# Performance work log

Hardware: AMD Instinct MI355X
Metric: run time of the kernel (lower is better)

## Reference

```python
import jax, jax.numpy as jnp
import numpy as np
import math

N = 8192
F_DIM = 128
ALPHA_SLOPE = 0.2  # LeakyReLU negative slope from __init__ alpha


def setup_inputs() -> dict:
    key = jax.random.key(0)
    k1, k2, k3, k4, k5 = jax.random.split(key, 5)
    inp = jax.random.normal(k1, (N, F_DIM), dtype=jnp.float32)
    adj = (jax.random.uniform(k2, (N, N)) < 0.02).astype(jnp.float32)
    adj = adj.at[jnp.arange(N), jnp.arange(N)].set(1.0)
    h0 = jax.random.normal(k3, (N, F_DIM), dtype=jnp.float32)
    W = jax.random.normal(k4, (F_DIM, F_DIM), dtype=jnp.float32) * (1.414 * math.sqrt(6.0 / (2 * F_DIM)))
    a = jax.random.normal(k5, (2 * F_DIM, 1), dtype=jnp.float32) * (1.414 * math.sqrt(6.0 / (2 * F_DIM + 1)))
    return {"inp": inp, "adj": adj, "h0": h0, "W": W, "a": a,
            "lamda": 0.5, "alpha_mix": 0.1, "l": 1}


def reference(inp, adj, h0, W, a, lamda, alpha_mix, l):
    # h = inp @ W  -> (N, F)
    h = inp @ W
    # score(i,j) = leakyrelu([h_i, h_j] @ a) = leakyrelu(h_i@a1 + h_j@a2)
    # avoids materializing the O(N^2 * 2F) a_input tensor of the original
    f1 = h @ a[:F_DIM, 0]   # (N,)
    f2 = h @ a[F_DIM:, 0]   # (N,)
    e = jax.nn.leaky_relu(f1[:, None] + f2[None, :], negative_slope=ALPHA_SLOPE)  # (N, N)
    e = jnp.where(adj > 0, e, jnp.float32(-1e12))
    attention = jax.nn.softmax(e, axis=1)
    # dropout skipped (inference / training=False)
    hi = attention @ inp                      # (N, F) -- note: aggregates inp, not h
    support = (1.0 - alpha_mix) * hi + alpha_mix * h0
    theta = min(1.0, math.log(lamda / l + 1.0))
    output = theta * (support @ W) + (1.0 - theta) * support + inp
    return output
```

## Files before the change

### kernel.cpp

```cpp
#include <hip/hip_runtime.h>
#include <math.h>

#define N 8192
#define F 128
#define SLOPE 0.2f
#define SEGCAP 96
#define RPB 4

typedef float f4v __attribute__((ext_vector_type(4)));

__device__ __forceinline__ float lrelu(float x) { return x > 0.0f ? x : SLOPE * x; }

__device__ __forceinline__ f4v ntload(const float* p) {
    return __builtin_nontemporal_load(reinterpret_cast<const f4v*>(p));
}

__device__ __forceinline__ int mbcnt64(unsigned long long m) {
    return __builtin_amdgcn_mbcnt_hi((unsigned)(m >> 32),
                                     __builtin_amdgcn_mbcnt_lo((unsigned)m, 0u));
}

__device__ __forceinline__ unsigned bf16pair(float a, float b) {
    unsigned ua = __builtin_bit_cast(unsigned, a);
    unsigned ub = __builtin_bit_cast(unsigned, b);
    ua = (ua + 0x7FFFu + ((ua >> 16) & 1u)) >> 16;
    ub = (ub + 0x7FFFu + ((ub >> 16) & 1u)) >> 16;
    return ua | (ub << 16);
}
__device__ __forceinline__ float bflo(unsigned u) {
    return __builtin_bit_cast(float, u << 16);
}
__device__ __forceinline__ float bfhi(unsigned u) {
    return __builtin_bit_cast(float, u & 0xFFFF0000u);
}

__global__ __launch_bounds__(256) void k_wa(const float* __restrict__ W,
                                            const float* __restrict__ a,
                                            float* __restrict__ Wa) {
    const int t = threadIdx.x;
    const int k = t & 127;
    const int half = t >> 7;
    const f4v* wr = reinterpret_cast<const f4v*>(W + k * F);
    const f4v* av = reinterpret_cast<const f4v*>(a + half * F);
    float s = 0.f;
    #pragma unroll
    for (int q = 0; q < 32; ++q) {
        const f4v w = wr[q], aa = av[q];
        s += (w[0] * aa[0] + w[1] * aa[1]) + (w[2] * aa[2] + w[3] * aa[3]);
    }
    Wa[t] = s;
}

__global__ __launch_bounds__(256, 8) void k_main(const float* __restrict__ adj,
                                                 const float* __restrict__ inp,
                                                 const float* __restrict__ Wa,
                                                 float* __restrict__ f1,
                                                 float* __restrict__ f2,
                                                 unsigned* __restrict__ inpb,
                                                 int* __restrict__ nzidx,
                                                 int* __restrict__ nzcnt) {
    __shared__ int s_seg[4][SEGCAP];
    const int bid = blockIdx.x;
    const int wv = threadIdx.x >> 6;
    const int lane = threadIdx.x & 63;

    if (bid < N) {
        const float* base = adj + (size_t)bid * N + wv * 2048 + lane * 4;
        f4v v[8];
        #pragma unroll
        for (int u = 0; u < 8; ++u) v[u] = ntload(base + u * 256);

        int cnt = 0;
        #pragma unroll
        for (int u = 0; u < 8; ++u) {
            const int col0 = wv * 2048 + u * 256 + lane * 4;
            #pragma unroll
            for (int c = 0; c < 4; ++c) {
                const bool nz = v[u][c] > 0.f;
                const unsigned long long m = __ballot(nz);
                const int pos = mbcnt64(m);
                int p = cnt + pos;
                if (p > SEGCAP - 1) p = SEGCAP - 1;
                if (nz) s_seg[wv][p] = col0 + c;
                cnt += (int)__popcll(m);
            }
        }
        const int M = cnt > SEGCAP ? SEGCAP : cnt;
        int* seg = nzidx + ((size_t)bid * 4 + wv) * SEGCAP;
        for (int t2 = lane; t2 < M; t2 += 64) seg[t2] = s_seg[wv][t2];
        if (lane == 0) nzcnt[bid * 4 + wv] = M;
    } else {
        const int i = (bid - N) * 4 + wv;
        const float2 xv = *reinterpret_cast<const float2*>(inp + (size_t)i * F + 2 * lane);
        const float2 w1v = *reinterpret_cast<const float2*>(Wa + 2 * lane);
        const float2 w2v = *reinterpret_cast<const float2*>(Wa + F + 2 * lane);
        float v1 = xv.x * w1v.x + xv.y * w1v.y;
        float v2 = xv.x * w2v.x + xv.y * w2v.y;
        #pragma unroll
        for (int off = 32; off; off >>= 1) {
            v1 += __shfl_xor(v1, off);
            v2 += __shfl_xor(v2, off);
        }
        if (lane == 0) { f1[i] = v1; f2[i] = v2; }
        inpb[i * 64 + lane] = bf16pair(xv.x, xv.y);
    }
}

__global__ __launch_bounds__(256, 4) void k_agg(const int* __restrict__ nzidx,
                                                const int* __restrict__ nzcnt,
                                                const unsigned* __restrict__ inpb,
                                                const float* __restrict__ inp,
                                                const float* __restrict__ h0,
                                                const float* __restrict__ W,
                                                const float* __restrict__ f1,
                                                const float* __restrict__ f2,
                                                const float* __restrict__ lamda_p,
                                                const float* __restrict__ alpha_p,
                                                const int* __restrict__ l_p,
                                                float* __restrict__ out) {
    const int r0 = blockIdx.x * RPB;
    const int t = threadIdx.x;
    const int lane = t & 63;
    const int wv = t >> 6;
    const int i = r0 + wv;

    __shared__ int   s_j[RPB][400];
    __shared__ float s_w[RPB][400];
    __shared__ float s_sup[RPB][F];
    __shared__ float s_dot[RPB][F];

    const float f1i = f1[i];

    int cnts[4], jA[4], jB[4];
    float sA[4], sB[4];
    float mx = -1e30f;
    #pragma unroll
    for (int s = 0; s < 4; ++s) {
        cnts[s] = nzcnt[i * 4 + s];
        const int* seg = nzidx + ((size_t)i * 4 + s) * SEGCAP;
        jA[s] = (lane < cnts[s]) ? seg[lane] : -1;
        jB[s] = (64 + lane < cnts[s]) ? seg[64 + lane] : -1;
        sA[s] = (jA[s] >= 0) ? lrelu(f1i + f2[jA[s]]) : -1e30f;
        sB[s] = (jB[s] >= 0) ? lrelu(f1i + f2[jB[s]]) : -1e30f;
        mx = fmaxf(mx, fmaxf(sA[s], sB[s]));
    }
    #pragma unroll
    for (int off = 32; off; off >>= 1) mx = fmaxf(mx, __shfl_xor(mx, off));

    int total = 0;
    float wlane = 0.f;
    #pragma unroll
    for (int s = 0; s < 4; ++s) {
        float w1 = 0.f, w2 = 0.f;
        if (jA[s] >= 0) {
            w1 = __expf(sA[s] - mx);
            s_j[wv][total + lane] = jA[s];
            s_w[wv][total + lane] = w1;
        }
        if (jB[s] >= 0) {
            w2 = __expf(sB[s] - mx);
            s_j[wv][total + 64 + lane] = jB[s];
            s_w[wv][total + 64 + lane] = w2;
        }
        wlane += w1 + w2;
        total += cnts[s];
    }
    if (lane < 8) { s_j[wv][total + lane] = 0; s_w[wv][total + lane] = 0.f; }
    float wsum = wlane;
    #pragma unroll
    for (int off = 32; off; off >>= 1) wsum += __shfl_xor(wsum, off);

    float acc_e = 0.f, acc_o = 0.f;
    for (int e = 0; e < total; e += 8) {
        const int4 jv0 = *reinterpret_cast<const int4*>(&s_j[wv][e]);
        const int4 jv1 = *reinterpret_cast<const int4*>(&s_j[wv][e + 4]);
        const f4v  wq0 = *reinterpret_cast<const f4v*>(&s_w[wv][e]);
        const f4v  wq1 = *reinterpret_cast<const f4v*>(&s_w[wv][e + 4]);
        const unsigned a0 = inpb[(size_t)jv0.x * 64 + lane];
        const unsigned a1 = inpb[(size_t)jv0.y * 64 + lane];
        const unsigned a2 = inpb[(size_t)jv0.z * 64 + lane];
        const unsigned a3 = inpb[(size_t)jv0.w * 64 + lane];
        const unsigned a4 = inpb[(size_t)jv1.x * 64 + lane];
        const unsigned a5 = inpb[(size_t)jv1.y * 64 + lane];
        const unsigned a6 = inpb[(size_t)jv1.z * 64 + lane];
        const unsigned a7 = inpb[(size_t)jv1.w * 64 + lane];
        acc_e = fmaf(wq0[0], bflo(a0), acc_e); acc_o = fmaf(wq0[0], bfhi(a0), acc_o);
        acc_e = fmaf(wq0[1], bflo(a1), acc_e); acc_o = fmaf(wq0[1], bfhi(a1), acc_o);
        acc_e = fmaf(wq0[2], bflo(a2), acc_e); acc_o = fmaf(wq0[2], bfhi(a2), acc_o);
        acc_e = fmaf(wq0[3], bflo(a3), acc_e); acc_o = fmaf(wq0[3], bfhi(a3), acc_o);
        acc_e = fmaf(wq1[0], bflo(a4), acc_e); acc_o = fmaf(wq1[0], bfhi(a4), acc_o);
        acc_e = fmaf(wq1[1], bflo(a5), acc_e); acc_o = fmaf(wq1[1], bfhi(a5), acc_o);
        acc_e = fmaf(wq1[2], bflo(a6), acc_e); acc_o = fmaf(wq1[2], bfhi(a6), acc_o);
        acc_e = fmaf(wq1[3], bflo(a7), acc_e); acc_o = fmaf(wq1[3], bfhi(a7), acc_o);
    }

    const float inv = 1.0f / wsum;
    const float alpha = *alpha_p;
    const float2 hv = *reinterpret_cast<const float2*>(h0 + (size_t)i * F + 2 * lane);
    const float sup_e = (1.0f - alpha) * (acc_e * inv) + alpha * hv.x;
    const float sup_o = (1.0f - alpha) * (acc_o * inv) + alpha * hv.y;
    s_sup[wv][2 * lane]     = sup_e;
    s_sup[wv][2 * lane + 1] = sup_o;
    __syncthreads();

    const int c = t & 127;
    const int h = t >> 7;
    float d0 = 0.f, d1 = 0.f, d2 = 0.f, d3 = 0.f;
    const int k0 = 64 * h;
    #pragma unroll 4
    for (int k = k0; k < k0 + 64; ++k) {
        const float wk = W[k * F + c];
        d0 = fmaf(s_sup[0][k], wk, d0);
        d1 = fmaf(s_sup[1][k], wk, d1);
        d2 = fmaf(s_sup[2][k], wk, d2);
        d3 = fmaf(s_sup[3][k], wk, d3);
    }
    if (h == 0) {
        s_dot[0][c] = d0; s_dot[1][c] = d1; s_dot[2][c] = d2; s_dot[3][c] = d3;
    }
    __syncthreads();
    if (h == 1) {
        const float lam = *lamda_p;
        const float th = fminf(1.0f, logf(lam / (float)(*l_p) + 1.0f));
        const float dr[4] = { d0 + s_dot[0][c], d1 + s_dot[1][c],
                              d2 + s_dot[2][c], d3 + s_dot[3][c] };
        #pragma unroll
        for (int r = 0; r < RPB; ++r) {
            const size_t o = (size_t)(r0 + r) * F + c;
            out[o] = th * dr[r] + (1.0f - th) * s_sup[r][c] + inp[o];
        }
    }
}

extern "C" void kernel_launch(void* const* d_in, const int* in_sizes, int n_in,
                              void* d_out, int out_size, void* d_ws, size_t ws_size,
                              hipStream_t stream) {
    const float* inp   = (const float*)d_in[0];
    const float* adj   = (const float*)d_in[1];
    const float* h0    = (const float*)d_in[2];
    const float* W     = (const float*)d_in[3];
    const float* a     = (const float*)d_in[4];
    const float* lamda = (const float*)d_in[5];
    const float* alpha = (const float*)d_in[6];
    const int*   l     = (const int*)d_in[7];
    float* out = (float*)d_out;

    float* ws = (float*)d_ws;
    float*    Wa    = ws;
    float*    f1    = ws + 256;
    float*    f2    = ws + 256 + N;
    int*      nzcnt = (int*)(ws + 256 + 2 * N);
    int*      nzidx = (int*)(ws + 49408);
    unsigned* inpb  = (unsigned*)(ws + 3195136);

    hipLaunchKernelGGL(k_wa, dim3(1), dim3(256), 0, stream, W, a, Wa);
    hipLaunchKernelGGL(k_main, dim3(N + 2048), dim3(256), 0, stream,
                       adj, inp, Wa, f1, f2, inpb, nzidx, nzcnt);
    hipLaunchKernelGGL(k_agg, dim3(N / RPB), dim3(256), 0, stream,
                       nzidx, nzcnt, inpb, inp, h0, W, f1, f2, lamda, alpha, l, out);
}
```

Before: 90.62 us.

## Fuse adjacency scan with attention aggregation, one row per block

New measurement: 93.36 us. +3.0%, slower.

```diff
diff --git a/kernel.cpp b/kernel.cpp
--- a/kernel.cpp
+++ b/kernel.cpp
@@ -5,7 +5,7 @@
 #define F 128
 #define SLOPE 0.2f
 #define SEGCAP 96
-#define RPB 4
+#define SEGPAD 104
 
 typedef float f4v __attribute__((ext_vector_type(4)));
 
@@ -51,127 +51,99 @@
     Wa[t] = s;
 }
 
-__global__ __launch_bounds__(256, 8) void k_main(const float* __restrict__ adj,
-                                                 const float* __restrict__ inp,
-                                                 const float* __restrict__ Wa,
-                                                 float* __restrict__ f1,
-                                                 float* __restrict__ f2,
-                                                 unsigned* __restrict__ inpb,
-                                                 int* __restrict__ nzidx,
-                                                 int* __restrict__ nzcnt) {
-    __shared__ int s_seg[4][SEGCAP];
-    const int bid = blockIdx.x;
+__global__ __launch_bounds__(256) void k_pre(const float* __restrict__ inp,
+                                             const float* __restrict__ Wa,
+                                             float* __restrict__ f1,
+                                             float* __restrict__ f2,
+                                             unsigned* __restrict__ inpb) {
+    const int lane = threadIdx.x & 63;
     const int wv = threadIdx.x >> 6;
-    const int lane = threadIdx.x & 63;
-
-    if (bid < N) {
-        const float* base = adj + (size_t)bid * N + wv * 2048 + lane * 4;
-        f4v v[8];
-        #pragma unroll
-        for (int u = 0; u < 8; ++u) v[u] = ntload(base + u * 256);
-
-        int cnt = 0;
-        #pragma unroll
-        for (int u = 0; u < 8; ++u) {
-            const int col0 = wv * 2048 + u * 256 + lane * 4;
-            #pragma unroll
-            for (int c = 0; c < 4; ++c) {
-                const bool nz = v[u][c] > 0.f;
-                const unsigned long long m = __ballot(nz);
-                const int pos = mbcnt64(m);
-                int p = cnt + pos;
-                if (p > SEGCAP - 1) p = SEGCAP - 1;
-                if (nz) s_seg[wv][p] = col0 + c;
-                cnt += (int)__popcll(m);
-            }
-        }
-        const int M = cnt > SEGCAP ? SEGCAP : cnt;
-        int* seg = nzidx + ((size_t)bid * 4 + wv) * SEGCAP;
-        for (int t2 = lane; t2 < M; t2 += 64) seg[t2] = s_seg[wv][t2];
-        if (lane == 0) nzcnt[bid * 4 + wv] = M;
-    } else {
-        const int i = (bid - N) * 4 + wv;
-        const float2 xv = *reinterpret_cast<const float2*>(inp + (size_t)i * F + 2 * lane);
-        const float2 w1v = *reinterpret_cast<const float2*>(Wa + 2 * lane);
-        const float2 w2v = *reinterpret_cast<const float2*>(Wa + F + 2 * lane);
-        float v1 = xv.x * w1v.x + xv.y * w1v.y;
-        float v2 = xv.x * w2v.x + xv.y * w2v.y;
-        #pragma unroll
-        for (int off = 32; off; off >>= 1) {
-            v1 += __shfl_xor(v1, off);
-            v2 += __shfl_xor(v2, off);
-        }
-        if (lane == 0) { f1[i] = v1; f2[i] = v2; }
-        inpb[i * 64 + lane] = bf16pair(xv.x, xv.y);
-    }
-}
-
-__global__ __launch_bounds__(256, 4) void k_agg(const int* __restrict__ nzidx,
-                                                const int* __restrict__ nzcnt,
-                                                const unsigned* __restrict__ inpb,
-                                                const float* __restrict__ inp,
-                                                const float* __restrict__ h0,
-                                                const float* __restrict__ W,
-                                                const float* __restrict__ f1,
-                                                const float* __restrict__ f2,
-                                                const float* __restrict__ lamda_p,
-                                                const float* __restrict__ alpha_p,
-                                                const int* __restrict__ l_p,
-                                                float* __restrict__ out) {
-    const int r0 = blockIdx.x * RPB;
+    const int i = blockIdx.x * 4 + wv;
+    const float2 xv = *reinterpret_cast<const float2*>(inp + (size_t)i * F + 2 * lane);
+    const float2 w1v = *reinterpret_cast<const float2*>(Wa + 2 * lane);
+    const float2 w2v = *reinterpret_cast<const float2*>(Wa + F + 2 * lane);
+    float v1 = xv.x * w1v.x + xv.y * w1v.y;
+    float v2 = xv.x * w2v.x + xv.y * w2v.y;
+    #pragma unroll
+    for (int off = 32; off; off >>= 1) {
+        v1 += __shfl_xor(v1, off);
+        v2 += __shfl_xor(v2, off);
+    }
+    if (lane == 0) { f1[i] = v1; f2[i] = v2; }
+    inpb[i * 64 + lane] = bf16pair(xv.x, xv.y);
+}
+
+__global__ __launch_bounds__(256, 8) void k_fused(const float* __restrict__ adj,
+                                                  const unsigned* __restrict__ inpb,
+                                                  const float* __restrict__ inp,
+                                                  const float* __restrict__ h0,
+                                                  const float* __restrict__ W,
+                                                  const float* __restrict__ f1,
+                                                  const float* __restrict__ f2,
+                                                  const float* __restrict__ lamda_p,
+                                                  const float* __restrict__ alpha_p,
+                                                  const int* __restrict__ l_p,
+                                                  float* __restrict__ out) {
+    const int i = blockIdx.x;
     const int t = threadIdx.x;
     const int lane = t & 63;
     const int wv = t >> 6;
-    const int i = r0 + wv;
-
-    __shared__ int   s_j[RPB][400];
-    __shared__ float s_w[RPB][400];
-    __shared__ float s_sup[RPB][F];
-    __shared__ float s_dot[RPB][F];
+
+    __shared__ int   s_j[4][SEGPAD];
+    __shared__ float s_w[4][SEGPAD];
+    __shared__ float s_acc[4][F];
+    __shared__ float s_sup[F];
+    __shared__ float s_dot[F];
+    __shared__ float s_mx[4];
+    __shared__ float s_ws[4];
+
+    const float* base = adj + (size_t)i * N + wv * 2048 + lane * 4;
+    f4v v[8];
+    #pragma unroll
+    for (int u = 0; u < 8; ++u) v[u] = ntload(base + u * 256);
+
+    int cnt = 0;
+    #pragma unroll
+    for (int u = 0; u < 8; ++u) {
+        const int col0 = wv * 2048 + u * 256 + lane * 4;
+        #pragma unroll
+        for (int c = 0; c < 4; ++c) {
+            const bool nz = v[u][c] > 0.f;
+            const unsigned long long m = __ballot(nz);
+            const int pos = mbcnt64(m);
+            int p = cnt + pos;
+            if (p > SEGCAP - 1) p = SEGCAP - 1;
+            if (nz) s_j[wv][p] = col0 + c;
+            cnt += (int)__popcll(m);
+        }
+    }
+    const int M = cnt > SEGCAP ? SEGCAP : cnt;
 
     const float f1i = f1[i];
-
-    int cnts[4], jA[4], jB[4];
-    float sA[4], sB[4];
-    float mx = -1e30f;
-    #pragma unroll
-    for (int s = 0; s < 4; ++s) {
-        cnts[s] = nzcnt[i * 4 + s];
-        const int* seg = nzidx + ((size_t)i * 4 + s) * SEGCAP;
-        jA[s] = (lane < cnts[s]) ? seg[lane] : -1;
-        jB[s] = (64 + lane < cnts[s]) ? seg[64 + lane] : -1;
-        sA[s] = (jA[s] >= 0) ? lrelu(f1i + f2[jA[s]]) : -1e30f;
-        sB[s] = (jB[s] >= 0) ? lrelu(f1i + f2[jB[s]]) : -1e30f;
-        mx = fmaxf(mx, fmaxf(sA[s], sB[s]));
-    }
+    const int jA = (lane < M) ? s_j[wv][lane] : -1;
+    const int jB = (64 + lane < M) ? s_j[wv][64 + lane] : -1;
+    float sA = -1e30f, sB = -1e30f;
+    if (jA >= 0) sA = lrelu(f1i + f2[jA]);
+    if (jB >= 0) sB = lrelu(f1i + f2[jB]);
+    float mx = fmaxf(sA, sB);
     #pragma unroll
     for (int off = 32; off; off >>= 1) mx = fmaxf(mx, __shfl_xor(mx, off));
-
-    int total = 0;
-    float wlane = 0.f;
-    #pragma unroll
-    for (int s = 0; s < 4; ++s) {
-        float w1 = 0.f, w2 = 0.f;
-        if (jA[s] >= 0) {
-            w1 = __expf(sA[s] - mx);
-            s_j[wv][total + lane] = jA[s];
-            s_w[wv][total + lane] = w1;
-        }
-        if (jB[s] >= 0) {
-            w2 = __expf(sB[s] - mx);
-            s_j[wv][total + 64 + lane] = jB[s];
-            s_w[wv][total + 64 + lane] = w2;
-        }
-        wlane += w1 + w2;
-        total += cnts[s];
-    }
-    if (lane < 8) { s_j[wv][total + lane] = 0; s_w[wv][total + lane] = 0.f; }
-    float wsum = wlane;
-    #pragma unroll
-    for (int off = 32; off; off >>= 1) wsum += __shfl_xor(wsum, off);
+    if (lane == 0) s_mx[wv] = mx;
+    __syncthreads();
+    const float bm = fmaxf(fmaxf(s_mx[0], s_mx[1]), fmaxf(s_mx[2], s_mx[3]));
+
+    float wA = 0.f, wB = 0.f;
+    if (jA >= 0) { wA = __expf(sA - bm); s_w[wv][lane] = wA; }
+    if (jB >= 0) { wB = __expf(sB - bm); s_w[wv][64 + lane] = wB; }
+    if (lane < 8) { s_j[wv][M + lane] = 0; s_w[wv][M + lane] = 0.f; }
+    float wl = wA + wB;
+    #pragma unroll
+    for (int off = 32; off; off >>= 1) wl += __shfl_xor(wl, off);
+    if (lane == 0) s_ws[wv] = wl;
 
     float acc_e = 0.f, acc_o = 0.f;
-    for (int e = 0; e < total; e += 8) {
+    const int MP = (M + 7) & ~7;
+    for (int e = 0; e < MP; e += 8) {
         const int4 jv0 = *reinterpret_cast<const int4*>(&s_j[wv][e]);
         const int4 jv1 = *reinterpret_cast<const int4*>(&s_j[wv][e + 4]);
         const f4v  wq0 = *reinterpret_cast<const f4v*>(&s_w[wv][e]);
@@ -193,42 +165,34 @@
         acc_e = fmaf(wq1[2], bflo(a6), acc_e); acc_o = fmaf(wq1[2], bfhi(a6), acc_o);
         acc_e = fmaf(wq1[3], bflo(a7), acc_e); acc_o = fmaf(wq1[3], bfhi(a7), acc_o);
     }
-
-    const float inv = 1.0f / wsum;
-    const float alpha = *alpha_p;
-    const float2 hv = *reinterpret_cast<const float2*>(h0 + (size_t)i * F + 2 * lane);
-    const float sup_e = (1.0f - alpha) * (acc_e * inv) + alpha * hv.x;
-    const float sup_o = (1.0f - alpha) * (acc_o * inv) + alpha * hv.y;
-    s_sup[wv][2 * lane]     = sup_e;
-    s_sup[wv][2 * lane + 1] = sup_o;
+    s_acc[wv][2 * lane]     = acc_e;
+    s_acc[wv][2 * lane + 1] = acc_o;
+    __syncthreads();
+
+    if (t < F) {
+        const float tot = (s_acc[0][t] + s_acc[1][t]) + (s_acc[2][t] + s_acc[3][t]);
+        const float wtot = (s_ws[0] + s_ws[1]) + (s_ws[2] + s_ws[3]);
+        const float hi = tot / wtot;
+        const float alpha = *alpha_p;
+        s_sup[t] = (1.0f - alpha) * hi + alpha * h0[(size_t)i * F + t];
+    }
     __syncthreads();
 
     const int c = t & 127;
     const int h = t >> 7;
-    float d0 = 0.f, d1 = 0.f, d2 = 0.f, d3 = 0.f;
+    float dot = 0.f;
     const int k0 = 64 * h;
     #pragma unroll 4
-    for (int k = k0; k < k0 + 64; ++k) {
-        const float wk = W[k * F + c];
-        d0 = fmaf(s_sup[0][k], wk, d0);
-        d1 = fmaf(s_sup[1][k], wk, d1);
-        d2 = fmaf(s_sup[2][k], wk, d2);
-        d3 = fmaf(s_sup[3][k], wk, d3);
-    }
-    if (h == 0) {
-        s_dot[0][c] = d0; s_dot[1][c] = d1; s_dot[2][c] = d2; s_dot[3][c] = d3;
-    }
+    for (int k = k0; k < k0 + 64; ++k) dot = fmaf(s_sup[k], W[k * F + c], dot);
+    if (h == 0) s_dot[c] = dot;
     __syncthreads();
     if (h == 1) {
+        const float d = dot + s_dot[c];
         const float lam = *lamda_p;
         const float th = fminf(1.0f, logf(lam / (float)(*l_p) + 1.0f));
-        const float dr[4] = { d0 + s_dot[0][c], d1 + s_dot[1][c],
-                              d2 + s_dot[2][c], d3 + s_dot[3][c] };
-        #pragma unroll
-        for (int r = 0; r < RPB; ++r) {
-            const size_t o = (size_t)(r0 + r) * F + c;
-            out[o] = th * dr[r] + (1.0f - th) * s_sup[r][c] + inp[o];
-        }
+        const float sup = s_sup[c];
+        const size_t o = (size_t)i * F + c;
+        out[o] = th * d + (1.0f - th) * sup + inp[o];
     }
 }
 
@@ -246,16 +210,13 @@
     float* out = (float*)d_out;
 
     float* ws = (float*)d_ws;
-    float*    Wa    = ws;
-    float*    f1    = ws + 256;
-    float*    f2    = ws + 256 + N;
-    int*      nzcnt = (int*)(ws + 256 + 2 * N);
-    int*      nzidx = (int*)(ws + 49408);
-    unsigned* inpb  = (unsigned*)(ws + 3195136);
+    float*    Wa   = ws;
+    float*    f1   = ws + 256;
+    float*    f2   = ws + 256 + N;
+    unsigned* inpb = (unsigned*)(ws + 256 + 2 * N + 64);
 
     hipLaunchKernelGGL(k_wa, dim3(1), dim3(256), 0, stream, W, a, Wa);
-    hipLaunchKernelGGL(k_main, dim3(N + 2048), dim3(256), 0, stream,
-                       adj, inp, Wa, f1, f2, inpb, nzidx, nzcnt);
-    hipLaunchKernelGGL(k_agg, dim3(N / RPB), dim3(256), 0, stream,
-                       nzidx, nzcnt, inpb, inp, h0, W, f1, f2, lamda, alpha, l, out);
-}
+    hipLaunchKernelGGL(k_pre, dim3(N / 4), dim3(256), 0, stream, inp, Wa, f1, f2, inpb);
+    hipLaunchKernelGGL(k_fused, dim3(N), dim3(256), 0, stream,
+                       adj, inpb, inp, h0, W, f1, f2, lamda, alpha, l, out);
+}
```
